# Kernel tuning notes

Hardware: AMD Instinct MI355X
Metric: run time of the kernel (lower is better)

## Reference

```python
import jax, jax.numpy as jnp
import numpy as np
import jax.scipy.signal as jss

SX, SY, C, K = 256, 256, 3, 10
C0 = [0, 0, 0, 1, 1, 1, 2, 2, 2, 0]
C1 = [[0, 1, 2, 9], [3, 4, 5], [6, 7, 8]]
DD, DT, SIGMA = 5, 0.2, 0.65

_KX = jnp.array([[-1., 0., 1.], [-2., 0., 2.], [-1., 0., 1.]])
_KY = _KX.T


def _conv2(A, Kf):
    # zero-padded 'same' 2D true convolution, vmapped over channel axis
    return jax.vmap(lambda a: jss.convolve2d(a, Kf, mode='same'), in_axes=2, out_axes=2)(A)


def sobel(A):
    # (X, Y, c) -> (X, Y, 2, c): [sobel_y, sobel_x] stacked on axis 2 (FlowLenia convention)
    return jnp.concatenate([_conv2(A, _KY)[:, :, None, :], _conv2(A, _KX)[:, :, None, :]], axis=2)


def growth(U, m, s):
    # bell(U,m,s)*2 - 1
    return jnp.exp(-((U - m) / s) ** 2 / 2.) * 2. - 1.


def get_kernels_fft(R, r, a, w, b):
    # FlowLenia kernel construction: ring distance -> smooth cutoff * sum-of-bumps, normalized, fft2(fftshift)
    mid = SX // 2
    xs = jnp.arange(-mid, mid, dtype=jnp.float32)
    D = jnp.sqrt(xs[:, None] ** 2 + xs[None, :] ** 2)            # (X, Y)
    Dk = D[..., None] / ((R + 15.) * r)                          # (X, Y, k)
    ker = (b * jnp.exp(-(Dk[..., None] - a) ** 2 / w)).sum(-1)   # (X, Y, k)
    sig = 0.5 * (jnp.tanh(-(Dk - 1.) * 10. / 2.) + 1.)           # sigmoid(-(D-1)*10)
    Kk = sig * ker
    nK = Kk / Kk.sum(axis=(0, 1), keepdims=True)
    return jnp.fft.fft2(jnp.fft.fftshift(nK, axes=(0, 1)), axes=(0, 1))


def _rt_apply(A, F):
    # Reintegration tracking with 'wall' border: flow-driven mass redistribution over a (2dd+1)^2 neighborhood
    ii = jnp.arange(SX, dtype=jnp.float32)
    pos = jnp.stack(jnp.meshgrid(ii, ii, indexing='ij'), axis=-1) + 0.5   # (X, Y, 2) cell centers
    ma = DD - SIGMA                                   # max flow magnitude
    mu = pos[..., None] + jnp.clip(DT * F, -ma, ma)   # (X, Y, 2, C) target centers
    mu = jnp.clip(mu, SIGMA, SX - SIGMA)              # wall border
    offs = jnp.arange(-DD, DD + 1)
    gx, gy = jnp.meshgrid(offs, offs, indexing='ij')
    dxs, dys = gx.reshape(-1), gy.reshape(-1)
    clip_hi = min(1., 2. * SIGMA)

    def step(dx, dy):
        Ar = jnp.roll(A, (dx, dy), axis=(0, 1))
        mur = jnp.roll(mu, (dx, dy), axis=(0, 1))
        dpmu = jnp.abs(pos[..., None] - mur)                                  # (X, Y, 2, C)
        sz = 0.5 - dpmu + SIGMA
        area = jnp.prod(jnp.clip(sz, 0., clip_hi), axis=2) / (4. * SIGMA ** 2)  # (X, Y, C)
        return Ar * area

    return jax.vmap(step)(dxs, dys).sum(axis=0)


def setup_inputs() -> dict:
    key = jax.random.key(0)
    ks = jax.random.split(key, 9)
    A = jax.random.uniform(ks[0], (SX, SY, C), dtype=jnp.float32)
    R = jax.random.uniform(ks[1], (), minval=2.0, maxval=25.0)
    r = jax.random.uniform(ks[2], (K,), minval=0.2, maxval=1.0)
    m = jax.random.uniform(ks[3], (K,), minval=0.05, maxval=0.5)
    s = jax.random.uniform(ks[4], (K,), minval=0.001, maxval=0.18)
    h = jax.random.uniform(ks[5], (K,), minval=0.01, maxval=1.0)
    a = jax.random.uniform(ks[6], (K, 3), minval=0.0, maxval=1.0)
    b = jax.random.uniform(ks[7], (K, 3), minval=0.001, maxval=1.0)
    w = jax.random.uniform(ks[8], (K, 3), minval=0.01, maxval=0.5)
    return dict(A=A, R=R, r=r, m=m, s=s, h=h, a=a, b=b, w=w)


def reference(A, R, r, m, s, h, a, b, w):
    fK = get_kernels_fft(R, r, a, w, b)                       # (X, Y, k) complex
    fA = jnp.fft.fft2(A, axes=(0, 1))
    fAk = fA[:, :, jnp.array(C0)]                             # (X, Y, k)
    U = jnp.real(jnp.fft.ifft2(fK * fAk, axes=(0, 1)))        # (X, Y, k)
    U = growth(U, m, s) * h
    U = jnp.dstack([U[:, :, C1[c]].sum(axis=-1) for c in range(C)])  # (X, Y, C)
    nabla_U = sobel(U)                                        # (X, Y, 2, C)
    nabla_A = sobel(A.sum(axis=-1, keepdims=True))            # (X, Y, 2, 1)
    alpha = jnp.clip((A[:, :, None, :] / C) ** 2, 0., 1.)     # (X, Y, 1, C)
    F = nabla_U * (1. - alpha) - nabla_A * alpha              # (X, Y, 2, C)
    return _rt_apply(A, F)
```

## Files before the change

### kernel.cpp

```cpp
#include <hip/hip_runtime.h>

#define NPIX 65536

#define WS_APLANE 0
#define WS_ASUM   (3*NPIX)
#define WS_KOFF   (4*NPIX)
#define WS_MUX    (4*NPIX)
#define WS_MUY    (7*NPIX)
#define WS_UACC   (14*NPIX)
#define WS_ROWS   (24*NPIX)
#define WS_X1RE   (25*NPIX)
#define WS_X1IM   (38*NPIX)
#define WS_X2RE   (51*NPIX)
#define WS_X2IM   (64*NPIX)
#define WS_END    (77*NPIX)

__global__ void k_prep(const float* __restrict__ A,
                       const float* __restrict__ R_, const float* __restrict__ r_,
                       const float* __restrict__ a_, const float* __restrict__ b_,
                       const float* __restrict__ w_, float* __restrict__ ws) {
    int bid = blockIdx.x;
    int t = threadIdx.x;
    if (bid < 256) {
        int idx = bid * 256 + t;
        float a0 = A[idx*3+0], a1 = A[idx*3+1], a2 = A[idx*3+2];
        ws[WS_APLANE + idx]          = a0;
        ws[WS_APLANE + NPIX + idx]   = a1;
        ws[WS_APLANE + 2*NPIX + idx] = a2;
        ws[WS_ASUM + idx] = a0 + a1 + a2;
        return;
    }
    __shared__ float red[4];
    int bk = bid - 256;
    int k = bk >> 8;
    int i = bk & 255;
    int wid = t >> 6, lane = t & 63;
    float R = R_[0];
    float denom = (R + 15.0f) * r_[k];
    int di = i - 128, dj = t - 128;
    float D  = sqrtf((float)(di*di + dj*dj));
    float Dk = D / denom;
    float v = 0.0f;
    if (Dk <= 3.0f) {
        float ker = 0.0f;
        #pragma unroll
        for (int tt = 0; tt < 3; ++tt) {
            float d = Dk - a_[k*3+tt];
            ker += b_[k*3+tt] * expf(-((d*d) / w_[k*3+tt]));
        }
        float sig = 1.0f / (1.0f + expf(10.0f * (Dk - 1.0f)));
        v = sig * ker;
    }
    int iw = (i + 128) & 255;
    int jw = (t + 128) & 255;
    ws[WS_KOFF + k*NPIX + iw*256 + jw] = v;
    float s = v;
    #pragma unroll
    for (int off = 32; off; off >>= 1) s += __shfl_xor(s, off);
    if (lane == 0) red[wid] = s;
    __syncthreads();
    if (t == 0) ws[WS_ROWS + k*256 + i] = red[0] + red[1] + red[2] + red[3];
}

__device__ __forceinline__ void fft256_core(float* __restrict__ re, float* __restrict__ im,
                                            const float* __restrict__ twr,
                                            const float* __restrict__ twi, int lane) {
    #pragma unroll
    for (int s = 1; s <= 8; ++s) {
        int h = 1 << (s - 1);
        #pragma unroll
        for (int b = 0; b < 2; ++b) {
            int idx = b*64 + lane;
            int pos = idx & (h - 1);
            int g   = idx >> (s - 1);
            int i0 = (g << s) + pos;
            int i1 = i0 + h;
            int tj = pos << (8 - s);
            float wr = twr[tj], wi = twi[tj];
            float xr = re[i1], xi = im[i1];
            float br = fmaf(xr, wr, -xi*wi);
            float bi = fmaf(xr, wi,  xi*wr);
            float ar = re[i0], ai = im[i0];
            re[i0] = ar + br; im[i0] = ai + bi;
            re[i1] = ar - br; im[i1] = ai - bi;
        }
    }
}

__device__ __forceinline__ void build_tw(float* twr, float* twi, int t, float sgn) {
    if (t < 128) {
        float ang = (float)t * 0.0245436930f;
        twr[t] = cosf(ang);
        twi[t] = sgn * sinf(ang);
    }
}

__device__ __forceinline__ void store_t4(float* __restrict__ dst, const float* __restrict__ buf,
                                         int off, int t, int lb) {
    float4 v;
    v.x = buf[0*512 + off + t];
    v.y = buf[1*512 + off + t];
    v.z = buf[2*512 + off + t];
    v.w = buf[3*512 + off + t];
    *(float4*)&dst[t*256 + lb] = v;
}

__global__ __launch_bounds__(256) void fft_fwd_packed(float* __restrict__ ws) {
    __shared__ float buf[4*512];
    __shared__ float twr[128], twi[128];
    int p  = blockIdx.x >> 6;
    int lb = (blockIdx.x & 63) * 4;
    int wid = threadIdx.x >> 6, lane = threadIdx.x & 63;
    int t = threadIdx.x;
    build_tw(twr, twi, t, -1.0f);
    int f = 2*p, g = 2*p + 1;
    const float* frow = ws + ((f < 3) ? (WS_APLANE + f*NPIX) : (WS_KOFF + (f-3)*NPIX))
                      + (lb + wid)*256;
    const float* grow = (g < 13)
        ? ws + ((g < 3) ? (WS_APLANE + g*NPIX) : (WS_KOFF + (g-3)*NPIX)) + (lb + wid)*256
        : nullptr;
    float* re = &buf[wid*512];
    float* im = re + 256;
    #pragma unroll
    for (int e = 0; e < 4; ++e) {
        int idx = e*64 + lane;
        int dst = __brev(idx) >> 24;
        re[dst] = frow[idx];
        im[dst] = grow ? grow[idx] : 0.0f;
    }
    __syncthreads();
    fft256_core(re, im, twr, twi, lane);
    __syncthreads();
    int u2 = (256 - t) & 255;
    float4 Fre, Fim, Gre, Gim;
    float* pF[4] = {&Fre.x, &Fim.x, &Gre.x, &Gim.x};
    #pragma unroll
    for (int l = 0; l < 4; ++l) {
        float zr1 = buf[l*512 + t],  zi1 = buf[l*512 + 256 + t];
        float zr2 = buf[l*512 + u2], zi2 = buf[l*512 + 256 + u2];
        pF[0][l] = 0.5f*(zr1 + zr2);
        pF[1][l] = 0.5f*(zi1 - zi2);
        pF[2][l] = 0.5f*(zi1 + zi2);
        pF[3][l] = 0.5f*(zr2 - zr1);
    }
    *(float4*)&ws[WS_X1RE + f*NPIX + t*256 + lb] = Fre;
    *(float4*)&ws[WS_X1IM + f*NPIX + t*256 + lb] = Fim;
    if (g < 13) {
        *(float4*)&ws[WS_X1RE + g*NPIX + t*256 + lb] = Gre;
        *(float4*)&ws[WS_X1IM + g*NPIX + t*256 + lb] = Gim;
    }
}

__global__ __launch_bounds__(256) void fft_fwd_cplx(float* __restrict__ ws) {
    __shared__ float buf[4*512];
    __shared__ float twr[128], twi[128];
    int p  = blockIdx.x >> 6;
    int lb = (blockIdx.x & 63) * 4;
    int wid = threadIdx.x >> 6, lane = threadIdx.x & 63;
    int t = threadIdx.x;
    build_tw(twr, twi, t, -1.0f);
    float* re = &buf[wid*512];
    float* im = re + 256;
    const float* rr = ws + WS_X1RE + p*NPIX + (lb + wid)*256;
    const float* ri = ws + WS_X1IM + p*NPIX + (lb + wid)*256;
    #pragma unroll
    for (int e = 0; e < 4; ++e) {
        int idx = e*64 + lane;
        int dst = __brev(idx) >> 24;
        re[dst] = rr[idx];
        im[dst] = ri[idx];
    }
    __syncthreads();
    fft256_core(re, im, twr, twi, lane);
    __syncthreads();
    store_t4(ws + WS_X2RE + p*NPIX, buf, 0,   t, lb);
    store_t4(ws + WS_X2IM + p*NPIX, buf, 256, t, lb);
}

__global__ __launch_bounds__(256) void ifft_mul_packed(float* __restrict__ ws) {
    __shared__ float buf[4*512];
    __shared__ float twr[128], twi[128];
    int j  = blockIdx.x >> 6;
    int lb = (blockIdx.x & 63) * 4;
    int wid = threadIdx.x >> 6, lane = threadIdx.x & 63;
    int t = threadIdx.x;
    build_tw(twr, twi, t, 1.0f);
    const int C0[10] = {0,0,0,1,1,1,2,2,2,0};
    int ka = 2*j, kb = 2*j + 1;
    int ca = C0[ka], cb = C0[kb];
    int rowoff = (lb + wid)*256;
    const float* arp = ws + WS_X2RE + ca*NPIX + rowoff;
    const float* aip = ws + WS_X2IM + ca*NPIX + rowoff;
    const float* krp = ws + WS_X2RE + (3+ka)*NPIX + rowoff;
    const float* kip = ws + WS_X2IM + (3+ka)*NPIX + rowoff;
    const float* brp = ws + WS_X2RE + cb*NPIX + rowoff;
    const float* bip = ws + WS_X2IM + cb*NPIX + rowoff;
    const float* lrp = ws + WS_X2RE + (3+kb)*NPIX + rowoff;
    const float* lip = ws + WS_X2IM + (3+kb)*NPIX + rowoff;
    float* re = &buf[wid*512];
    float* im = re + 256;
    #pragma unroll
    for (int e = 0; e < 4; ++e) {
        int idx = e*64 + lane;
        int dst = __brev(idx) >> 24;
        float ar = arp[idx], ai = aip[idx];
        float kr = krp[idx], ki = kip[idx];
        float uar = ar*kr - ai*ki;
        float uai = ar*ki + ai*kr;
        float br = brp[idx], bi = bip[idx];
        float lr = lrp[idx], li = lip[idx];
        float ubr = br*lr - bi*li;
        float ubi = br*li + bi*lr;
        re[dst] = uar - ubi;
        im[dst] = uai + ubr;
    }
    __syncthreads();
    fft256_core(re, im, twr, twi, lane);
    __syncthreads();
    store_t4(ws + WS_X1RE + j*NPIX, buf, 0,   t, lb);
    store_t4(ws + WS_X1IM + j*NPIX, buf, 256, t, lb);
}

__global__ __launch_bounds__(256) void ifft_real_packed(float* __restrict__ ws) {
    __shared__ float buf[4*512];
    __shared__ float twr[128], twi[128];
    int j  = blockIdx.x >> 6;
    int lb = (blockIdx.x & 63) * 4;
    int wid = threadIdx.x >> 6, lane = threadIdx.x & 63;
    int t = threadIdx.x;
    build_tw(twr, twi, t, 1.0f);
    float* re = &buf[wid*512];
    float* im = re + 256;
    const float* rr = ws + WS_X1RE + j*NPIX + (lb + wid)*256;
    const float* ri = ws + WS_X1IM + j*NPIX + (lb + wid)*256;
    #pragma unroll
    for (int e = 0; e < 4; ++e) {
        int idx = e*64 + lane;
        int dst = __brev(idx) >> 24;
        re[dst] = rr[idx];
        im[dst] = ri[idx];
    }
    __syncthreads();
    fft256_core(re, im, twr, twi, lane);
    __syncthreads();
    const float sc = 1.0f / 65536.0f;
    float4 va, vb;
    va.x = buf[0*512 + t] * sc;       vb.x = buf[0*512 + 256 + t] * sc;
    va.y = buf[1*512 + t] * sc;       vb.y = buf[1*512 + 256 + t] * sc;
    va.z = buf[2*512 + t] * sc;       vb.z = buf[2*512 + 256 + t] * sc;
    va.w = buf[3*512 + t] * sc;       vb.w = buf[3*512 + 256 + t] * sc;
    *(float4*)&ws[WS_UACC + (2*j)*NPIX   + t*256 + lb] = va;
    *(float4*)&ws[WS_UACC + (2*j+1)*NPIX + t*256 + lb] = vb;
}

__device__ inline void sobel_at(const float* __restrict__ p, int x, int y,
                                float& gy, float& gx) {
    float v[3][3];
    #pragma unroll
    for (int ii = -1; ii <= 1; ++ii)
        #pragma unroll
        for (int jj = -1; jj <= 1; ++jj) {
            int xx = x + ii, yy = y + jj;
            v[ii+1][jj+1] = (xx < 0 || xx > 255 || yy < 0 || yy > 255)
                            ? 0.0f : p[xx*256 + yy];
        }
    gy = (v[0][0] + 2.0f*v[0][1] + v[0][2]) - (v[2][0] + 2.0f*v[2][1] + v[2][2]);
    gx = (v[0][0] + 2.0f*v[1][0] + v[2][0]) - (v[0][2] + 2.0f*v[1][2] + v[2][2]);
}

__global__ __launch_bounds__(256) void growth_mu(float* __restrict__ ws,
                                                 const float* __restrict__ m_,
                                                 const float* __restrict__ s_,
                                                 const float* __restrict__ h_) {
    __shared__ float Ush[3][256];
    __shared__ float kinv[4];
    int b = blockIdx.x;
    int c = b >> 8;
    int x = b & 255;
    int t = threadIdx.x, wid = t >> 6, lane = t & 63;
    int nk = (c == 0) ? 4 : 3;
    if (wid < nk) {
        int k = (wid == 3) ? 9 : c*3 + wid;
        const float* rw = ws + WS_ROWS + k*256;
        float v = rw[lane] + rw[64+lane] + rw[128+lane] + rw[192+lane];
        #pragma unroll
        for (int off = 32; off; off >>= 1) v += __shfl_xor(v, off);
        if (lane == 0) kinv[wid] = 1.0f / v;
    }
    __syncthreads();
    const float* uacc = ws + WS_UACC;
    for (int rr = 0; rr < 3; ++rr) {
        int xr = x - 1 + rr;
        float outv = 0.0f;
        if (xr >= 0 && xr <= 255) {
            int idx = xr*256 + t;
            for (int kk = 0; kk < nk; ++kk) {
                int k = (kk == 3) ? 9 : c*3 + kk;
                float U = uacc[k*NPIX + idx] * kinv[kk];
                float z = (U - m_[k]) / s_[k];
                outv += h_[k] * (expf(-0.5f*z*z)*2.0f - 1.0f);
            }
        }
        Ush[rr][t] = outv;
    }
    __syncthreads();
    int y = t;
    float gyA, gxA;
    sobel_at(ws + WS_ASUM, x, y, gyA, gxA);
    float v[3][3];
    #pragma unroll
    for (int ii = -1; ii <= 1; ++ii)
        #pragma unroll
        for (int jj = -1; jj <= 1; ++jj) {
            int xx = x + ii, yy = y + jj;
            v[ii+1][jj+1] = (xx < 0 || xx > 255 || yy < 0 || yy > 255)
                            ? 0.0f : Ush[ii+1][yy];
        }
    float gy = (v[0][0] + 2.0f*v[0][1] + v[0][2]) - (v[2][0] + 2.0f*v[2][1] + v[2][2]);
    float gx = (v[0][0] + 2.0f*v[1][0] + v[2][0]) - (v[0][2] + 2.0f*v[1][2] + v[2][2]);
    float a = ws[WS_APLANE + c*NPIX + x*256 + y];
    float al = (a / 3.0f); al = al * al;
    al = fminf(fmaxf(al, 0.0f), 1.0f);
    float F0 = gy * (1.0f - al) - gyA * al;
    float F1 = gx * (1.0f - al) - gxA * al;
    float d0 = fminf(fmaxf(0.2f * F0, -4.35f), 4.35f);
    float d1 = fminf(fmaxf(0.2f * F1, -4.35f), 4.35f);
    ws[WS_MUX + c*NPIX + x*256 + y] = fminf(fmaxf((float)x + 0.5f + d0, 0.65f), 255.35f);
    ws[WS_MUY + c*NPIX + x*256 + y] = fminf(fmaxf((float)y + 0.5f + d1, 0.65f), 255.35f);
}

__global__ __launch_bounds__(256) void rt_apply_v2(const float* __restrict__ ws,
                                                   float* __restrict__ out) {
    __shared__ float sA[11*256], sX[11*256], sY[11*256];
    int b = blockIdx.x;
    int c = b >> 8;
    int x = b & 255;
    const float* ap = ws + WS_APLANE + c*NPIX;
    const float* mx = ws + WS_MUX + c*NPIX;
    const float* my = ws + WS_MUY + c*NPIX;
    int t = threadIdx.x;
    #pragma unroll
    for (int i = 0; i < 11; ++i) {
        int src = (((x - (i - 5)) & 255) << 8) + t;
        sA[i*256 + t] = ap[src];
        sX[i*256 + t] = mx[src];
        sY[i*256 + t] = my[src];
    }
    __syncthreads();
    int y = t;
    float px = (float)x + 0.5f, py = (float)y + 0.5f;
    float acc = 0.0f;
    #pragma unroll
    for (int dx = -5; dx <= 5; ++dx) {
        int rb = (dx + 5) * 256;
        for (int dy = -5; dy <= 5; ++dy) {
            int sy = (y - dy) & 255;
            float a  = sA[rb + sy];
            float ax = 1.15f - fabsf(px - sX[rb + sy]);
            float ay = 1.15f - fabsf(py - sY[rb + sy]);
            ax = fminf(fmaxf(ax, 0.0f), 1.0f);
            ay = fminf(fmaxf(ay, 0.0f), 1.0f);
            acc = fmaf(a, ax * ay, acc);
        }
    }
    out[(x*256 + y)*3 + c] = acc * (1.0f / (4.0f * 0.65f * 0.65f));
}

extern "C" void kernel_launch(void* const* d_in, const int* in_sizes, int n_in,
                              void* d_out, int out_size, void* d_ws, size_t ws_size,
                              hipStream_t stream) {
    const float* A = (const float*)d_in[0];
    const float* R = (const float*)d_in[1];
    const float* r = (const float*)d_in[2];
    const float* m = (const float*)d_in[3];
    const float* s = (const float*)d_in[4];
    const float* h = (const float*)d_in[5];
    const float* a = (const float*)d_in[6];
    const float* b = (const float*)d_in[7];
    const float* w = (const float*)d_in[8];
    float* ws  = (float*)d_ws;
    float* out = (float*)d_out;

    k_prep<<<256 + 2560, 256, 0, stream>>>(A, R, r, a, b, w, ws);
    fft_fwd_packed<<<7*64, 256, 0, stream>>>(ws);
    fft_fwd_cplx<<<13*64, 256, 0, stream>>>(ws);
    ifft_mul_packed<<<5*64, 256, 0, stream>>>(ws);
    ifft_real_packed<<<5*64, 256, 0, stream>>>(ws);
    growth_mu<<<768, 256, 0, stream>>>(ws, m, s, h);
    rt_apply_v2<<<768, 256, 0, stream>>>(ws, out);
}
```

Before: 122.5 us.

## Fuse kernel generation into row FFT and exploit Hermitian/real-even kernel symmetry

Drops the separate prep kernel. The first row-FFT pass now computes the ring kernels and reads A directly. Because the kernels are real and even, their spectra are real and symmetric, so only the real part and half the columns are computed and stored. The multiply stage then reconstructs the conjugate half for the A spectra. Growth and reintegration read A directly and compute the channel sum inline, removing the plane and sum scratch buffers. This cuts one launch and a large share of the column-FFT work and memory traffic, at the cost of more complex indexing and some thread idling.

```diff
diff --git a/kernel.cpp b/kernel.cpp
--- a/kernel.cpp
+++ b/kernel.cpp
@@ -2,65 +2,18 @@
 
 #define NPIX 65536
 
-#define WS_APLANE 0
-#define WS_ASUM   (3*NPIX)
-#define WS_KOFF   (4*NPIX)
-#define WS_MUX    (4*NPIX)
-#define WS_MUY    (7*NPIX)
-#define WS_UACC   (14*NPIX)
-#define WS_ROWS   (24*NPIX)
-#define WS_X1RE   (25*NPIX)
-#define WS_X1IM   (38*NPIX)
-#define WS_X2RE   (51*NPIX)
-#define WS_X2IM   (64*NPIX)
-#define WS_END    (77*NPIX)
-
-__global__ void k_prep(const float* __restrict__ A,
-                       const float* __restrict__ R_, const float* __restrict__ r_,
-                       const float* __restrict__ a_, const float* __restrict__ b_,
-                       const float* __restrict__ w_, float* __restrict__ ws) {
-    int bid = blockIdx.x;
-    int t = threadIdx.x;
-    if (bid < 256) {
-        int idx = bid * 256 + t;
-        float a0 = A[idx*3+0], a1 = A[idx*3+1], a2 = A[idx*3+2];
-        ws[WS_APLANE + idx]          = a0;
-        ws[WS_APLANE + NPIX + idx]   = a1;
-        ws[WS_APLANE + 2*NPIX + idx] = a2;
-        ws[WS_ASUM + idx] = a0 + a1 + a2;
-        return;
-    }
-    __shared__ float red[4];
-    int bk = bid - 256;
-    int k = bk >> 8;
-    int i = bk & 255;
-    int wid = t >> 6, lane = t & 63;
-    float R = R_[0];
-    float denom = (R + 15.0f) * r_[k];
-    int di = i - 128, dj = t - 128;
-    float D  = sqrtf((float)(di*di + dj*dj));
-    float Dk = D / denom;
-    float v = 0.0f;
-    if (Dk <= 3.0f) {
-        float ker = 0.0f;
-        #pragma unroll
-        for (int tt = 0; tt < 3; ++tt) {
-            float d = Dk - a_[k*3+tt];
-            ker += b_[k*3+tt] * expf(-((d*d) / w_[k*3+tt]));
-        }
-        float sig = 1.0f / (1.0f + expf(10.0f * (Dk - 1.0f)));
-        v = sig * ker;
-    }
-    int iw = (i + 128) & 255;
-    int jw = (t + 128) & 255;
-    ws[WS_KOFF + k*NPIX + iw*256 + jw] = v;
-    float s = v;
-    #pragma unroll
-    for (int off = 32; off; off >>= 1) s += __shfl_xor(s, off);
-    if (lane == 0) red[wid] = s;
-    __syncthreads();
-    if (t == 0) ws[WS_ROWS + k*256 + i] = red[0] + red[1] + red[2] + red[3];
-}
+#define OX1ARE(c) ((0  + (c))*NPIX)
+#define OX1AIM(c) ((3  + (c))*NPIX)
+#define OX1K(k)   ((6  + (k))*NPIX)
+#define OX2ARE(c) ((16 + (c))*NPIX)
+#define OX2AIM(c) ((19 + (c))*NPIX)
+#define OX2K(k)   ((22 + (k))*NPIX)
+#define OX3RE(j)  ((32 + (j))*NPIX)
+#define OX3IM(j)  ((37 + (j))*NPIX)
+#define OU(k)     ((42 + (k))*NPIX)
+#define OMUX(c)   ((52 + (c))*NPIX)
+#define OMUY(c)   ((55 + (c))*NPIX)
+#define OROWS     (58*NPIX)
 
 __device__ __forceinline__ void fft256_core(float* __restrict__ re, float* __restrict__ im,
                                             const float* __restrict__ twr,
@@ -105,7 +58,33 @@
     *(float4*)&dst[t*256 + lb] = v;
 }
 
-__global__ __launch_bounds__(256) void fft_fwd_packed(float* __restrict__ ws) {
+struct KP { float rden, a0,a1,a2, b0,b1,b2, iw0,iw1,iw2; };
+
+__device__ __forceinline__ void load_kp(KP& kp, int k, float R,
+        const float* __restrict__ r_, const float* __restrict__ a_,
+        const float* __restrict__ b_, const float* __restrict__ w_) {
+    kp.rden = 1.0f / ((R + 15.0f) * r_[k]);
+    kp.a0 = a_[k*3+0]; kp.a1 = a_[k*3+1]; kp.a2 = a_[k*3+2];
+    kp.b0 = b_[k*3+0]; kp.b1 = b_[k*3+1]; kp.b2 = b_[k*3+2];
+    kp.iw0 = 1.0f/w_[k*3+0]; kp.iw1 = 1.0f/w_[k*3+1]; kp.iw2 = 1.0f/w_[k*3+2];
+}
+
+__device__ __forceinline__ float kval(int di, int dj, const KP& kp) {
+    float D  = sqrtf((float)(di*di + dj*dj));
+    float Dk = D * kp.rden;
+    if (Dk > 3.0f) return 0.0f;
+    float d0 = Dk - kp.a0, d1 = Dk - kp.a1, d2 = Dk - kp.a2;
+    float ker = kp.b0*expf(-(d0*d0)*kp.iw0)
+              + kp.b1*expf(-(d1*d1)*kp.iw1)
+              + kp.b2*expf(-(d2*d2)*kp.iw2);
+    float sig = 1.0f / (1.0f + expf(10.0f*(Dk - 1.0f)));
+    return sig * ker;
+}
+
+__global__ __launch_bounds__(256) void fwd_rows(const float* __restrict__ A,
+        const float* __restrict__ R_, const float* __restrict__ r_,
+        const float* __restrict__ a_, const float* __restrict__ b_,
+        const float* __restrict__ w_, float* __restrict__ ws) {
     __shared__ float buf[4*512];
     __shared__ float twr[128], twi[128];
     int p  = blockIdx.x >> 6;
@@ -113,71 +92,146 @@
     int wid = threadIdx.x >> 6, lane = threadIdx.x & 63;
     int t = threadIdx.x;
     build_tw(twr, twi, t, -1.0f);
-    int f = 2*p, g = 2*p + 1;
-    const float* frow = ws + ((f < 3) ? (WS_APLANE + f*NPIX) : (WS_KOFF + (f-3)*NPIX))
-                      + (lb + wid)*256;
-    const float* grow = (g < 13)
-        ? ws + ((g < 3) ? (WS_APLANE + g*NPIX) : (WS_KOFF + (g-3)*NPIX)) + (lb + wid)*256
-        : nullptr;
+    int iw = lb + wid;
     float* re = &buf[wid*512];
     float* im = re + 256;
+
+    int fa, fb;
+    switch (p) {
+        case 0:  fa = 0;  fb = 1;  break;
+        case 1:  fa = 2;  fb = 12; break;
+        case 2:  fa = 3;  fb = 4;  break;
+        case 3:  fa = 5;  fb = 6;  break;
+        case 4:  fa = 7;  fb = 8;  break;
+        case 5:  fa = 9;  fb = 10; break;
+        default: fa = 11; fb = -1; break;
+    }
+    bool aA = (fa < 3);
+    bool bA = (fb >= 0 && fb < 3);
+    float R = R_[0];
+    int di = ((iw + 128) & 255) - 128;
+    KP kpa, kpb;
+    if (!aA)      load_kp(kpa, fa - 3, R, r_, a_, b_, w_);
+    if (fb >= 3)  load_kp(kpb, fb - 3, R, r_, a_, b_, w_);
+    float sum_a = 0.0f, sum_b = 0.0f;
     #pragma unroll
     for (int e = 0; e < 4; ++e) {
         int idx = e*64 + lane;
         int dst = __brev(idx) >> 24;
-        re[dst] = frow[idx];
-        im[dst] = grow ? grow[idx] : 0.0f;
+        int dj  = ((idx + 128) & 255) - 128;
+        float vf, vg;
+        if (aA) vf = A[(iw*256 + idx)*3 + fa];
+        else    { vf = kval(di, dj, kpa); sum_a += vf; }
+        if (fb < 0)      vg = 0.0f;
+        else if (bA)     vg = A[(iw*256 + idx)*3 + fb];
+        else             { vg = kval(di, dj, kpb); sum_b += vg; }
+        re[dst] = vf;
+        im[dst] = vg;
+    }
+    if (!aA) {
+        float s = sum_a;
+        #pragma unroll
+        for (int off = 32; off; off >>= 1) s += __shfl_xor(s, off);
+        if (lane == 0) ws[OROWS + (fa - 3)*256 + iw] = s;
+    }
+    if (fb >= 3) {
+        float s = sum_b;
+        #pragma unroll
+        for (int off = 32; off; off >>= 1) s += __shfl_xor(s, off);
+        if (lane == 0) ws[OROWS + (fb - 3)*256 + iw] = s;
     }
     __syncthreads();
     fft256_core(re, im, twr, twi, lane);
     __syncthreads();
-    int u2 = (256 - t) & 255;
-    float4 Fre, Fim, Gre, Gim;
-    float* pF[4] = {&Fre.x, &Fim.x, &Gre.x, &Gim.x};
-    #pragma unroll
-    for (int l = 0; l < 4; ++l) {
-        float zr1 = buf[l*512 + t],  zi1 = buf[l*512 + 256 + t];
-        float zr2 = buf[l*512 + u2], zi2 = buf[l*512 + 256 + u2];
-        pF[0][l] = 0.5f*(zr1 + zr2);
-        pF[1][l] = 0.5f*(zi1 - zi2);
-        pF[2][l] = 0.5f*(zi1 + zi2);
-        pF[3][l] = 0.5f*(zr2 - zr1);
-    }
-    *(float4*)&ws[WS_X1RE + f*NPIX + t*256 + lb] = Fre;
-    *(float4*)&ws[WS_X1IM + f*NPIX + t*256 + lb] = Fim;
-    if (g < 13) {
-        *(float4*)&ws[WS_X1RE + g*NPIX + t*256 + lb] = Gre;
-        *(float4*)&ws[WS_X1IM + g*NPIX + t*256 + lb] = Gim;
-    }
-}
-
-__global__ __launch_bounds__(256) void fft_fwd_cplx(float* __restrict__ ws) {
+    if (t <= 128) {
+        if (p <= 1) {
+            int u2 = (256 - t) & 255;
+            float4 Fre, Fim, Gre, Gim;
+            float* pF[4] = {&Fre.x, &Fim.x, &Gre.x, &Gim.x};
+            #pragma unroll
+            for (int l = 0; l < 4; ++l) {
+                float zr1 = buf[l*512 + t],  zi1 = buf[l*512 + 256 + t];
+                float zr2 = buf[l*512 + u2], zi2 = buf[l*512 + 256 + u2];
+                pF[0][l] = 0.5f*(zr1 + zr2);
+                pF[1][l] = 0.5f*(zi1 - zi2);
+                pF[2][l] = 0.5f*(zi1 + zi2);
+                pF[3][l] = 0.5f*(zr2 - zr1);
+            }
+            if (p == 0) {
+                *(float4*)&ws[OX1ARE(0) + t*256 + lb] = Fre;
+                *(float4*)&ws[OX1AIM(0) + t*256 + lb] = Fim;
+                *(float4*)&ws[OX1ARE(1) + t*256 + lb] = Gre;
+                *(float4*)&ws[OX1AIM(1) + t*256 + lb] = Gim;
+            } else {
+                *(float4*)&ws[OX1ARE(2) + t*256 + lb] = Fre;
+                *(float4*)&ws[OX1AIM(2) + t*256 + lb] = Fim;
+                *(float4*)&ws[OX1K(9)   + t*256 + lb] = Gre;
+            }
+        } else {
+            float4 va, vb;
+            float* pV[2] = {&va.x, &vb.x};
+            #pragma unroll
+            for (int l = 0; l < 4; ++l) {
+                pV[0][l] = buf[l*512 + t];
+                pV[1][l] = buf[l*512 + 256 + t];
+            }
+            *(float4*)&ws[OX1K(fa - 3) + t*256 + lb] = va;
+            if (fb >= 0) *(float4*)&ws[OX1K(fb - 3) + t*256 + lb] = vb;
+        }
+    }
+}
+
+__global__ __launch_bounds__(256) void fwd_cols(float* __restrict__ ws) {
     __shared__ float buf[4*512];
     __shared__ float twr[128], twi[128];
-    int p  = blockIdx.x >> 6;
-    int lb = (blockIdx.x & 63) * 4;
+    int bid = blockIdx.x;
     int wid = threadIdx.x >> 6, lane = threadIdx.x & 63;
     int t = threadIdx.x;
     build_tw(twr, twi, t, -1.0f);
     float* re = &buf[wid*512];
     float* im = re + 256;
-    const float* rr = ws + WS_X1RE + p*NPIX + (lb + wid)*256;
-    const float* ri = ws + WS_X1IM + p*NPIX + (lb + wid)*256;
-    #pragma unroll
-    for (int e = 0; e < 4; ++e) {
-        int idx = e*64 + lane;
-        int dst = __brev(idx) >> 24;
-        re[dst] = rr[idx];
-        im[dst] = ri[idx];
-    }
-    __syncthreads();
-    fft256_core(re, im, twr, twi, lane);
-    __syncthreads();
-    store_t4(ws + WS_X2RE + p*NPIX, buf, 0,   t, lb);
-    store_t4(ws + WS_X2IM + p*NPIX, buf, 256, t, lb);
-}
-
-__global__ __launch_bounds__(256) void ifft_mul_packed(float* __restrict__ ws) {
+    if (bid < 99) {
+        int c  = bid / 33;
+        int ub = (bid % 33) * 4;
+        int u  = ub + wid; if (u > 128) u = 128;
+        const float* rr = ws + OX1ARE(c) + u*256;
+        const float* ri = ws + OX1AIM(c) + u*256;
+        #pragma unroll
+        for (int e = 0; e < 4; ++e) {
+            int idx = e*64 + lane;
+            int dst = __brev(idx) >> 24;
+            re[dst] = rr[idx];
+            im[dst] = ri[idx];
+        }
+        __syncthreads();
+        fft256_core(re, im, twr, twi, lane);
+        __syncthreads();
+        store_t4(ws + OX2ARE(c), buf, 0,   t, ub);
+        store_t4(ws + OX2AIM(c), buf, 256, t, ub);
+    } else {
+        int q  = (bid - 99) / 33;
+        int ub = ((bid - 99) % 33) * 4;
+        int u  = ub + wid; if (u > 128) u = 128;
+        const float* ra = ws + OX1K(2*q)     + u*256;
+        const float* rb = ws + OX1K(2*q + 1) + u*256;
+        #pragma unroll
+        for (int e = 0; e < 4; ++e) {
+            int idx = e*64 + lane;
+            int dst = __brev(idx) >> 24;
+            re[dst] = ra[idx];
+            im[dst] = rb[idx];
+        }
+        __syncthreads();
+        fft256_core(re, im, twr, twi, lane);
+        __syncthreads();
+        if (t <= 128) {
+            store_t4(ws + OX2K(2*q),     buf, 0,   t, ub);
+            store_t4(ws + OX2K(2*q + 1), buf, 256, t, ub);
+        }
+    }
+}
+
+__global__ __launch_bounds__(256) void inv_rows(float* __restrict__ ws) {
     __shared__ float buf[4*512];
     __shared__ float twr[128], twi[128];
     int j  = blockIdx.x >> 6;
@@ -185,43 +239,52 @@
     int wid = threadIdx.x >> 6, lane = threadIdx.x & 63;
     int t = threadIdx.x;
     build_tw(twr, twi, t, 1.0f);
-    const int C0[10] = {0,0,0,1,1,1,2,2,2,0};
     int ka = 2*j, kb = 2*j + 1;
-    int ca = C0[ka], cb = C0[kb];
-    int rowoff = (lb + wid)*256;
-    const float* arp = ws + WS_X2RE + ca*NPIX + rowoff;
-    const float* aip = ws + WS_X2IM + ca*NPIX + rowoff;
-    const float* krp = ws + WS_X2RE + (3+ka)*NPIX + rowoff;
-    const float* kip = ws + WS_X2IM + (3+ka)*NPIX + rowoff;
-    const float* brp = ws + WS_X2RE + cb*NPIX + rowoff;
-    const float* bip = ws + WS_X2IM + cb*NPIX + rowoff;
-    const float* lrp = ws + WS_X2RE + (3+kb)*NPIX + rowoff;
-    const float* lip = ws + WS_X2IM + (3+kb)*NPIX + rowoff;
+    int ca = (ka < 9) ? ka/3 : 0;
+    int cb = (kb < 9) ? kb/3 : 0;
+    int v  = lb + wid;
+    int vr = (256 - v) & 255;
+    int vf = (v <= 128) ? v : 256 - v;
+    const float* Aare_v = ws + OX2ARE(ca) + v*256;
+    const float* Aaim_v = ws + OX2AIM(ca) + v*256;
+    const float* Aare_r = ws + OX2ARE(ca) + vr*256;
+    const float* Aaim_r = ws + OX2AIM(ca) + vr*256;
+    const float* Bare_v = ws + OX2ARE(cb) + v*256;
+    const float* Baim_v = ws + OX2AIM(cb) + v*256;
+    const float* Bare_r = ws + OX2ARE(cb) + vr*256;
+    const float* Baim_r = ws + OX2AIM(cb) + vr*256;
+    const float* Ka = ws + OX2K(ka) + vf*256;
+    const float* Kb = ws + OX2K(kb) + vf*256;
     float* re = &buf[wid*512];
     float* im = re + 256;
     #pragma unroll
     for (int e = 0; e < 4; ++e) {
         int idx = e*64 + lane;
         int dst = __brev(idx) >> 24;
-        float ar = arp[idx], ai = aip[idx];
-        float kr = krp[idx], ki = kip[idx];
-        float uar = ar*kr - ai*ki;
-        float uai = ar*ki + ai*kr;
-        float br = brp[idx], bi = bip[idx];
-        float lr = lrp[idx], li = lip[idx];
-        float ubr = br*lr - bi*li;
-        float ubi = br*li + bi*lr;
+        bool hi = idx > 128;
+        int uf = hi ? 256 - idx : idx;
+        const float* pAr = hi ? Aare_r : Aare_v;
+        const float* pAi = hi ? Aaim_r : Aaim_v;
+        const float* pBr = hi ? Bare_r : Bare_v;
+        const float* pBi = hi ? Baim_r : Baim_v;
+        float ar = pAr[uf];
+        float ai = pAi[uf]; ai = hi ? -ai : ai;
+        float br = pBr[uf];
+        float bi = pBi[uf]; bi = hi ? -bi : bi;
+        float kva = Ka[uf], kvb = Kb[uf];
+        float uar = ar*kva, uai = ai*kva;
+        float ubr = br*kvb, ubi = bi*kvb;
         re[dst] = uar - ubi;
         im[dst] = uai + ubr;
     }
     __syncthreads();
     fft256_core(re, im, twr, twi, lane);
     __syncthreads();
-    store_t4(ws + WS_X1RE + j*NPIX, buf, 0,   t, lb);
-    store_t4(ws + WS_X1IM + j*NPIX, buf, 256, t, lb);
-}
-
-__global__ __launch_bounds__(256) void ifft_real_packed(float* __restrict__ ws) {
+    store_t4(ws + OX3RE(j), buf, 0,   t, lb);
+    store_t4(ws + OX3IM(j), buf, 256, t, lb);
+}
+
+__global__ __launch_bounds__(256) void inv_cols(float* __restrict__ ws) {
     __shared__ float buf[4*512];
     __shared__ float twr[128], twi[128];
     int j  = blockIdx.x >> 6;
@@ -231,8 +294,8 @@
     build_tw(twr, twi, t, 1.0f);
     float* re = &buf[wid*512];
     float* im = re + 256;
-    const float* rr = ws + WS_X1RE + j*NPIX + (lb + wid)*256;
-    const float* ri = ws + WS_X1IM + j*NPIX + (lb + wid)*256;
+    const float* rr = ws + OX3RE(j) + (lb + wid)*256;
+    const float* ri = ws + OX3IM(j) + (lb + wid)*256;
     #pragma unroll
     for (int e = 0; e < 4; ++e) {
         int idx = e*64 + lane;
@@ -249,30 +312,17 @@
     va.y = buf[1*512 + t] * sc;       vb.y = buf[1*512 + 256 + t] * sc;
     va.z = buf[2*512 + t] * sc;       vb.z = buf[2*512 + 256 + t] * sc;
     va.w = buf[3*512 + t] * sc;       vb.w = buf[3*512 + 256 + t] * sc;
-    *(float4*)&ws[WS_UACC + (2*j)*NPIX   + t*256 + lb] = va;
-    *(float4*)&ws[WS_UACC + (2*j+1)*NPIX + t*256 + lb] = vb;
-}
-
-__device__ inline void sobel_at(const float* __restrict__ p, int x, int y,
-                                float& gy, float& gx) {
-    float v[3][3];
-    #pragma unroll
-    for (int ii = -1; ii <= 1; ++ii)
-        #pragma unroll
-        for (int jj = -1; jj <= 1; ++jj) {
-            int xx = x + ii, yy = y + jj;
-            v[ii+1][jj+1] = (xx < 0 || xx > 255 || yy < 0 || yy > 255)
-                            ? 0.0f : p[xx*256 + yy];
-        }
-    gy = (v[0][0] + 2.0f*v[0][1] + v[0][2]) - (v[2][0] + 2.0f*v[2][1] + v[2][2]);
-    gx = (v[0][0] + 2.0f*v[1][0] + v[2][0]) - (v[0][2] + 2.0f*v[1][2] + v[2][2]);
-}
-
-__global__ __launch_bounds__(256) void growth_mu(float* __restrict__ ws,
+    *(float4*)&ws[OU(2*j)     + t*256 + lb] = va;
+    *(float4*)&ws[OU(2*j + 1) + t*256 + lb] = vb;
+}
+
+__global__ __launch_bounds__(256) void growth_mu(const float* __restrict__ A,
+                                                 float* __restrict__ ws,
                                                  const float* __restrict__ m_,
                                                  const float* __restrict__ s_,
                                                  const float* __restrict__ h_) {
     __shared__ float Ush[3][256];
+    __shared__ float As[3][256];
     __shared__ float kinv[4];
     int b = blockIdx.x;
     int c = b >> 8;
@@ -281,14 +331,23 @@
     int nk = (c == 0) ? 4 : 3;
     if (wid < nk) {
         int k = (wid == 3) ? 9 : c*3 + wid;
-        const float* rw = ws + WS_ROWS + k*256;
+        const float* rw = ws + OROWS + k*256;
         float v = rw[lane] + rw[64+lane] + rw[128+lane] + rw[192+lane];
         #pragma unroll
         for (int off = 32; off; off >>= 1) v += __shfl_xor(v, off);
         if (lane == 0) kinv[wid] = 1.0f / v;
     }
-    __syncthreads();
-    const float* uacc = ws + WS_UACC;
+    #pragma unroll
+    for (int rr = 0; rr < 3; ++rr) {
+        int xr = x - 1 + rr;
+        float sv = 0.0f;
+        if (xr >= 0 && xr <= 255) {
+            int base = (xr*256 + t)*3;
+            sv = A[base] + A[base + 1] + A[base + 2];
+        }
+        As[rr][t] = sv;
+    }
+    __syncthreads();
     for (int rr = 0; rr < 3; ++rr) {
         int xr = x - 1 + rr;
         float outv = 0.0f;
@@ -296,7 +355,7 @@
             int idx = xr*256 + t;
             for (int kk = 0; kk < nk; ++kk) {
                 int k = (kk == 3) ? 9 : c*3 + kk;
-                float U = uacc[k*NPIX + idx] * kinv[kk];
+                float U = ws[OU(k) + idx] * kinv[kk];
                 float z = (U - m_[k]) / s_[k];
                 outv += h_[k] * (expf(-0.5f*z*z)*2.0f - 1.0f);
             }
@@ -305,44 +364,45 @@
     }
     __syncthreads();
     int y = t;
-    float gyA, gxA;
-    sobel_at(ws + WS_ASUM, x, y, gyA, gxA);
-    float v[3][3];
-    #pragma unroll
-    for (int ii = -1; ii <= 1; ++ii)
-        #pragma unroll
-        for (int jj = -1; jj <= 1; ++jj) {
-            int xx = x + ii, yy = y + jj;
-            v[ii+1][jj+1] = (xx < 0 || xx > 255 || yy < 0 || yy > 255)
-                            ? 0.0f : Ush[ii+1][yy];
-        }
-    float gy = (v[0][0] + 2.0f*v[0][1] + v[0][2]) - (v[2][0] + 2.0f*v[2][1] + v[2][2]);
-    float gx = (v[0][0] + 2.0f*v[1][0] + v[2][0]) - (v[0][2] + 2.0f*v[1][2] + v[2][2]);
-    float a = ws[WS_APLANE + c*NPIX + x*256 + y];
+    float vA[3][3], vU[3][3];
+    #pragma unroll
+    for (int ii = 0; ii < 3; ++ii)
+        #pragma unroll
+        for (int jj = 0; jj < 3; ++jj) {
+            int yy = y - 1 + jj;
+            bool ok = (yy >= 0 && yy <= 255);
+            vA[ii][jj] = ok ? As[ii][yy]  : 0.0f;
+            vU[ii][jj] = ok ? Ush[ii][yy] : 0.0f;
+        }
+    float gyA = (vA[0][0] + 2.0f*vA[0][1] + vA[0][2]) - (vA[2][0] + 2.0f*vA[2][1] + vA[2][2]);
+    float gxA = (vA[0][0] + 2.0f*vA[1][0] + vA[2][0]) - (vA[0][2] + 2.0f*vA[1][2] + vA[2][2]);
+    float gy  = (vU[0][0] + 2.0f*vU[0][1] + vU[0][2]) - (vU[2][0] + 2.0f*vU[2][1] + vU[2][2]);
+    float gx  = (vU[0][0] + 2.0f*vU[1][0] + vU[2][0]) - (vU[0][2] + 2.0f*vU[1][2] + vU[2][2]);
+    float a = A[(x*256 + y)*3 + c];
     float al = (a / 3.0f); al = al * al;
     al = fminf(fmaxf(al, 0.0f), 1.0f);
     float F0 = gy * (1.0f - al) - gyA * al;
     float F1 = gx * (1.0f - al) - gxA * al;
     float d0 = fminf(fmaxf(0.2f * F0, -4.35f), 4.35f);
     float d1 = fminf(fmaxf(0.2f * F1, -4.35f), 4.35f);
-    ws[WS_MUX + c*NPIX + x*256 + y] = fminf(fmaxf((float)x + 0.5f + d0, 0.65f), 255.35f);
-    ws[WS_MUY + c*NPIX + x*256 + y] = fminf(fmaxf((float)y + 0.5f + d1, 0.65f), 255.35f);
-}
-
-__global__ __launch_bounds__(256) void rt_apply_v2(const float* __restrict__ ws,
+    ws[OMUX(c) + x*256 + y] = fminf(fmaxf((float)x + 0.5f + d0, 0.65f), 255.35f);
+    ws[OMUY(c) + x*256 + y] = fminf(fmaxf((float)y + 0.5f + d1, 0.65f), 255.35f);
+}
+
+__global__ __launch_bounds__(256) void rt_apply_v2(const float* __restrict__ A,
+                                                   const float* __restrict__ ws,
                                                    float* __restrict__ out) {
     __shared__ float sA[11*256], sX[11*256], sY[11*256];
     int b = blockIdx.x;
     int c = b >> 8;
     int x = b & 255;
-    const float* ap = ws + WS_APLANE + c*NPIX;
-    const float* mx = ws + WS_MUX + c*NPIX;
-    const float* my = ws + WS_MUY + c*NPIX;
+    const float* mx = ws + OMUX(c);
+    const float* my = ws + OMUY(c);
     int t = threadIdx.x;
     #pragma unroll
     for (int i = 0; i < 11; ++i) {
         int src = (((x - (i - 5)) & 255) << 8) + t;
-        sA[i*256 + t] = ap[src];
+        sA[i*256 + t] = A[src*3 + c];
         sX[i*256 + t] = mx[src];
         sY[i*256 + t] = my[src];
     }
@@ -381,11 +441,10 @@
     float* ws  = (float*)d_ws;
     float* out = (float*)d_out;
 
-    k_prep<<<256 + 2560, 256, 0, stream>>>(A, R, r, a, b, w, ws);
-    fft_fwd_packed<<<7*64, 256, 0, stream>>>(ws);
-    fft_fwd_cplx<<<13*64, 256, 0, stream>>>(ws);
-    ifft_mul_packed<<<5*64, 256, 0, stream>>>(ws);
-    ifft_real_packed<<<5*64, 256, 0, stream>>>(ws);
-    growth_mu<<<768, 256, 0, stream>>>(ws, m, s, h);
-    rt_apply_v2<<<768, 256, 0, stream>>>(ws, out);
-}
+    fwd_rows<<<7*64, 256, 0, stream>>>(A, R, r, a, b, w, ws);
+    fwd_cols<<<99 + 165, 256, 0, stream>>>(ws);
+    inv_rows<<<5*64, 256, 0, stream>>>(ws);
+    inv_cols<<<5*64, 256, 0, stream>>>(ws);
+    growth_mu<<<768, 256, 0, stream>>>(A, ws, m, s, h);
+    rt_apply_v2<<<768, 256, 0, stream>>>(A, ws, out);
+}
```

Measured after the change: 111.7 us, median of 2. 8.9% less time.
